# Performance work log

Measured on AMD Instinct MI355X. Metric: run time of the kernel, lower is better.

## Reference

```python
import jax, jax.numpy as jnp
import numpy as np

B, N, D, E, HEADS, HID = 8, 2048, 768, 4, 12, 3072
CAPF = 0.25
CAP = int(CAPF * N)  # 512 tokens per expert
DH = D // HEADS
EPS = 1e-5  # torch LayerNorm default
SCALE = 0.02


def _nested_masks(dim, n_exp):
    # expert e keeps the first dim // 2**e features (nested experts, MoNE)
    m = np.zeros((n_exp, dim), np.float32)
    for e in range(n_exp):
        m[e, : dim >> e] = 1.0
    return jnp.asarray(m)


def _ln(x, g, b):
    mu = x.mean(-1, keepdims=True)
    var = ((x - mu) ** 2).mean(-1, keepdims=True)
    return (x - mu) * jax.lax.rsqrt(var + EPS) * g + b


def setup_inputs() -> dict:
    key = jax.random.key(0)
    ks = jax.random.split(key, 8)
    return {
        "x": jax.random.normal(ks[0], (B, N, D), jnp.float32),
        "Wr": jax.random.normal(ks[1], (D, E), jnp.float32) * SCALE,
        "ln1_g": jnp.ones((D,), jnp.float32),
        "ln1_b": jnp.zeros((D,), jnp.float32),
        "ln2_g": jnp.ones((D,), jnp.float32),
        "ln2_b": jnp.zeros((D,), jnp.float32),
        "Wqkv": jax.random.normal(ks[2], (D, 3 * D), jnp.float32) * SCALE,
        "Wproj": jax.random.normal(ks[3], (D, D), jnp.float32) * SCALE,
        "bproj": jnp.zeros((D,), jnp.float32),
        "W1": jax.random.normal(ks[4], (D, HID), jnp.float32) * SCALE,
        "b1": jnp.zeros((HID,), jnp.float32),
        "W2": jax.random.normal(ks[5], (HID, D), jnp.float32) * SCALE,
        "b2": jnp.zeros((D,), jnp.float32),
    }


def reference(x, Wr, ln1_g, ln1_b, ln2_g, ln2_b, Wqkv, Wproj, bproj, W1, b1, W2, b2):
    mD = _nested_masks(D, E)[None, :, None, :]    # [1,E,1,D]
    mH = _nested_masks(HID, E)[None, :, None, :]  # [1,E,1,HID]

    # ---- expert-choice router ----
    probs = jax.nn.softmax(x @ Wr, axis=-1)                     # [B,N,E]
    gates, idx = jax.lax.top_k(probs.transpose(0, 2, 1), CAP)   # each [B,E,C]
    dispatch = jax.nn.one_hot(idx, N, dtype=x.dtype)            # [B,E,C,N]
    combine = dispatch * gates[..., None]                       # [B,E,C,N]

    # ---- attention branch (per-expert nested-masked attention) ----
    xn = _ln(x, ln1_g, ln1_b)
    xe = jnp.einsum('becn,bnd->becd', dispatch, xn)             # [B,E,C,D]
    qkv = (xe * mD) @ Wqkv                                      # input-masked linear
    q, k, v = jnp.split(qkv, 3, axis=-1)
    q, k, v = q * mD, k * mD, v * mD                            # nested output masks

    def to_heads(t):
        return t.reshape(B, E, CAP, HEADS, DH).transpose(0, 1, 3, 2, 4)  # [B,E,H,C,dh]

    q, k, v = to_heads(q), to_heads(k), to_heads(v)
    att = jax.nn.softmax(jnp.einsum('behcd,behkd->behck', q, k) * (DH ** -0.5), axis=-1)
    o = jnp.einsum('behck,behkd->behcd', att, v)
    o = o.transpose(0, 1, 3, 2, 4).reshape(B, E, CAP, D)
    ye = ((o @ Wproj) + bproj) * mD                             # masked proj
    x = x + jnp.einsum('becd,becn->bnd', ye, combine)           # combine back

    # ---- MLP branch (per-expert nested-masked MLP) ----
    xn2 = _ln(x, ln2_g, ln2_b)
    xe2 = jnp.einsum('becn,bnd->becd', dispatch, xn2)           # [B,E,C,D]
    h = jax.nn.gelu((((xe2 * mD) @ W1) + b1) * mH)              # [B,E,C,HID]
    y = ((h @ W2) + b2) * mD                                    # [B,E,C,D]
    x = x + jnp.einsum('becd,becn->bnd', y, combine)
    return x
```

## Files before the change

kernel.cpp:

```cpp
#include <hip/hip_runtime.h>
#include <stdint.h>

typedef uint16_t u16;
typedef uint32_t u32;
typedef uint64_t u64;
typedef float f32x4 __attribute__((ext_vector_type(4)));
typedef __bf16 bf16x8 __attribute__((ext_vector_type(8)));

#define DEVI __device__ __forceinline__

struct U4 { u32 a, b, c, d; };

DEVI u16 f2bf(float f) {
    u32 u = __builtin_bit_cast(u32, f);
    return (u16)((u + 0x7FFFu + ((u >> 16) & 1u)) >> 16);
}
DEVI float bf2f(u32 h) { return __builtin_bit_cast(float, h << 16); }
DEVI u32 cvt_pk_bf16(float lo, float hi) {
    u32 r;
    asm("v_cvt_pk_bf16_f32 %0, %1, %2" : "=v"(r) : "v"(lo), "v"(hi));
    return r;
}

DEVI float gelu_f(float x) {
    float u = 0.7978845608028654f * (x + 0.044715f * x * x * x);
    float t = exp2f(u * 2.885390081777927f);
    return x * (1.f - 1.f / (t + 1.f));
}

#define GLOAD_LDS16(gp, lp) \
    __builtin_amdgcn_global_load_lds((const __attribute__((address_space(1))) void*)(gp), \
                                     (__attribute__((address_space(3))) void*)(lp), 16, 0, 0)

struct WtJobs {
    const float* src[4]; u16* dst[4];
    int K[4], N[4], ntx[4], start[5];
};
__global__ __launch_bounds__(256) void wt_all_kernel(WtJobs a) {
    int j = 0;
#pragma unroll
    for (int k = 1; k < 4; k++) if ((int)blockIdx.x >= a.start[k]) j = k;
    const int local = blockIdx.x - a.start[j];
    const int N = a.N[j], K = a.K[j];
    const int n0 = (local % a.ntx[j]) * 32, k0 = (local / a.ntx[j]) * 32;
    const float* __restrict__ src = a.src[j];
    u16* __restrict__ dst = a.dst[j];
    __shared__ float tile[32][33];
    int tx = threadIdx.x & 31, ty = threadIdx.x >> 5;
#pragma unroll
    for (int i = 0; i < 32; i += 8)
        tile[ty + i][tx] = src[(size_t)(k0 + ty + i) * N + n0 + tx];
    __syncthreads();
#pragma unroll
    for (int i = 0; i < 32; i += 8)
        dst[(size_t)(n0 + ty + i) * K + k0 + tx] = f2bf(tile[tx][ty + i]);
}

__global__ __launch_bounds__(256) void routerln_kernel(const float* __restrict__ x,
                                                       const float* __restrict__ Wr,
                                                       const float* __restrict__ gw,
                                                       const float* __restrict__ bw,
                                                       float* __restrict__ probs,
                                                       u16* __restrict__ xn) {
    int wv = threadIdx.x >> 6, lane = threadIdx.x & 63;
    size_t t = (size_t)blockIdx.x * 4 + wv;
    const float4* xr = (const float4*)(x + t * 768);
    const float4* wr4 = (const float4*)Wr;
    float4 v[3]; float s = 0, s2 = 0, a0 = 0, a1 = 0, a2 = 0, a3 = 0;
#pragma unroll
    for (int i = 0; i < 3; i++) {
        int f4 = lane + 64 * i;
        v[i] = xr[f4];
        s += v[i].x + v[i].y + v[i].z + v[i].w;
        s2 += v[i].x * v[i].x + v[i].y * v[i].y + v[i].z * v[i].z + v[i].w * v[i].w;
#pragma unroll
        for (int jj = 0; jj < 4; jj++) {
            float xv = (jj == 0) ? v[i].x : (jj == 1) ? v[i].y : (jj == 2) ? v[i].z : v[i].w;
            float4 w = wr4[f4 * 4 + jj];
            a0 = fmaf(xv, w.x, a0); a1 = fmaf(xv, w.y, a1);
            a2 = fmaf(xv, w.z, a2); a3 = fmaf(xv, w.w, a3);
        }
    }
#pragma unroll
    for (int m = 1; m < 64; m <<= 1) {
        s += __shfl_xor(s, m); s2 += __shfl_xor(s2, m);
        a0 += __shfl_xor(a0, m); a1 += __shfl_xor(a1, m);
        a2 += __shfl_xor(a2, m); a3 += __shfl_xor(a3, m);
    }
    float mx = fmaxf(fmaxf(a0, a1), fmaxf(a2, a3));
    float e0 = expf(a0 - mx), e1 = expf(a1 - mx), e2 = expf(a2 - mx), e3 = expf(a3 - mx);
    float inv = 1.f / (e0 + e1 + e2 + e3);
    if (lane < 4) {
        float pv = (lane == 0) ? e0 : (lane == 1) ? e1 : (lane == 2) ? e2 : e3;
        int b = (int)(t >> 11), n = (int)(t & 2047);
        probs[(size_t)(b * 4 + lane) * 2048 + n] = pv * inv;
    }
    float mu = s * (1.f / 768.f);
    float var = s2 * (1.f / 768.f) - mu * mu;
    float rs = rsqrtf(var + 1e-5f);
    uint2* op = (uint2*)(xn + t * 768);
#pragma unroll
    for (int i = 0; i < 3; i++) {
        int j4 = (lane + 64 * i) * 4;
        float y0 = (v[i].x - mu) * rs * gw[j4 + 0] + bw[j4 + 0];
        float y1 = (v[i].y - mu) * rs * gw[j4 + 1] + bw[j4 + 1];
        float y2 = (v[i].z - mu) * rs * gw[j4 + 2] + bw[j4 + 2];
        float y3 = (v[i].w - mu) * rs * gw[j4 + 3] + bw[j4 + 3];
        uint2 o; o.x = cvt_pk_bf16(y0, y1); o.y = cvt_pk_bf16(y2, y3);
        op[lane + 64 * i] = o;
    }
}

__global__ __launch_bounds__(1024) void topk_kernel(const float* __restrict__ probs,
                                                    int* __restrict__ idx, float* __restrict__ gate,
                                                    int* __restrict__ rev) {
    int be = blockIdx.x; int b = be >> 2, e = be & 3;
    __shared__ u64 keys[2048];
    for (int n = threadIdx.x; n < 2048; n += 1024) {
        u32 p = __builtin_bit_cast(u32, probs[(size_t)be * 2048 + n]);
        keys[n] = ((u64)p << 32) | (u32)(2047 - n);
        rev[((size_t)b * 2048 + n) * 4 + e] = -1;
    }
    __syncthreads();
    for (int k = 2; k <= 2048; k <<= 1)
        for (int j = k >> 1; j > 0; j >>= 1) {
            for (int i = threadIdx.x; i < 2048; i += 1024) {
                int ixj = i ^ j;
                if (ixj > i) {
                    u64 a = keys[i], bb = keys[ixj];
                    bool up = ((i & k) == 0);
                    if (up ? (a < bb) : (a > bb)) { keys[i] = bb; keys[ixj] = a; }
                }
            }
            __syncthreads();
        }
    for (int c = threadIdx.x; c < 512; c += 1024) {
        u64 kk = keys[c];
        int n = 2047 - (int)(kk & 0xffffffffu);
        idx[be * 512 + c] = n;
        gate[be * 512 + c] = __builtin_bit_cast(float, (u32)(kk >> 32));
        rev[((size_t)b * 2048 + n) * 4 + e] = c;
    }
}

struct GemmJobs {
    const u16* A[4]; u16* C[4]; u16* VT[4]; const int* idx[4];
    const u16* BT; const float* bias;
    long sAb[4], sCb[4], sVb[4];
    int lda[4], ldc[4], nk[4], nmask[4], tps[4], tstart[4];
    int ldb;
};

template <int MODE>
__global__ __launch_bounds__(256) void gemm_kernel(GemmJobs a) {
    __shared__ __align__(16) char smem[2][16384];
    const int tid = threadIdx.x, wv = tid >> 6, lane = tid & 63;
    const int mt = blockIdx.y, bz = blockIdx.z;
    int e = 0;
#pragma unroll
    for (int k = 1; k < 4; k++) if ((int)blockIdx.x >= a.tstart[k]) e = k;
    const int local = blockIdx.x - a.tstart[e];
    int seg, ntl;
    if (MODE == 0) { seg = local / a.tps[e]; ntl = local - seg * a.tps[e]; }
    else { seg = 0; ntl = local; }
    const int nbase = seg * 768 + ntl * 128;
    const int lda = a.lda[e], ldc = a.ldc[e], nk = a.nk[e], nmask = a.nmask[e];
    const u16* Ap = a.A[e] + (long)bz * a.sAb[e];
    const int* ix = a.idx[e] ? (a.idx[e] + bz * 2048) : nullptr;

    auto stage = [&](int buf, int kt) {
        char* base = smem[buf] + ((wv >= 2) ? 8192 : 0);
        const int kb = kt * 32;
#pragma unroll
        for (int q = 0; q < 4; q++) {
            int i8 = (wv & 1) * 4 + q;
            int row = i8 * 16 + (lane >> 2);
            int clog = ((lane & 3) * 16) ^ ((row & 6) << 3);
            const u16* g;
            if (wv < 2) {
                int rs = ix ? ix[mt * 128 + row] : (mt * 128 + row);
                g = Ap + (long)rs * lda + kb;
            } else {
                g = a.BT + (long)(nbase + row) * a.ldb + kb;
            }
            GLOAD_LDS16((const char*)g + clog, base + i8 * 1024);
        }
    };

    f32x4 acc[4][4] = {};
    stage(0, 0);
    __syncthreads();
    int buf = 0;
    const int wr = wv >> 1, wc = wv & 1;
    const int cb = (lane >> 4) * 16;
    for (int kt = 0; kt < nk; kt++) {
        if (kt + 1 < nk) stage(buf ^ 1, kt + 1);
        const char* ab = smem[buf];
        const char* bb = smem[buf] + 8192;
        bf16x8 af[4], bfv[4];
#pragma unroll
        for (int mi = 0; mi < 4; mi++) {
            int r = wr * 64 + mi * 16 + (lane & 15);
            af[mi] = *(const bf16x8*)(ab + r * 64 + (cb ^ ((r & 6) << 3)));
        }
#pragma unroll
        for (int ni = 0; ni < 4; ni++) {
            int r = wc * 64 + ni * 16 + (lane & 15);
            bfv[ni] = *(const bf16x8*)(bb + r * 64 + (cb ^ ((r & 6) << 3)));
        }
#pragma unroll
        for (int mi = 0; mi < 4; mi++)
#pragma unroll
            for (int ni = 0; ni < 4; ni++)
                acc[mi][ni] = __builtin_amdgcn_mfma_f32_16x16x32_bf16(af[mi], bfv[ni], acc[mi][ni], 0, 0, 0);
        __syncthreads();
        buf ^= 1;
    }

    u16* Cb = a.C[e] + (long)bz * a.sCb[e];
    u16* Vb = (MODE == 0) ? (a.VT[e] + (long)bz * a.sVb[e]) : nullptr;
#pragma unroll
    for (int mi = 0; mi < 4; mi++) {
        const int r0 = mt * 128 + wr * 64 + mi * 16 + ((lane >> 4) << 2);
#pragma unroll
        for (int ni = 0; ni < 4; ni++) {
            const int colt = wc * 64 + ni * 16 + (lane & 15);
            const int nloc = ntl * 128 + colt;
            if (MODE == 0) {
                const bool act = nloc < nmask;
                if (seg < 2) {
                    u16* cp = Cb + (long)r0 * 1536 + seg * 768 + nloc;
#pragma unroll
                    for (int j = 0; j < 4; j++) cp[(long)j * 1536] = act ? f2bf(acc[mi][ni][j]) : (u16)0;
                } else {
                    uint2 pv;
                    if (act) { pv.x = cvt_pk_bf16(acc[mi][ni][0], acc[mi][ni][1]);
                               pv.y = cvt_pk_bf16(acc[mi][ni][2], acc[mi][ni][3]); }
                    else { pv.x = 0; pv.y = 0; }
                    *(uint2*)(Vb + (long)nloc * 512 + r0) = pv;
                }
            } else {
                const float bv = a.bias[nloc];
#pragma unroll
                for (int j = 0; j < 4; j++) {
                    float v = acc[mi][ni][j] + bv;
                    if (MODE == 2) v = gelu_f(v);
                    Cb[(long)(r0 + j) * ldc + nloc] = f2bf(v);
                }
            }
        }
    }
}

__global__ __launch_bounds__(256) void attn_kernel(const u16* __restrict__ qkv,
                                                   const u16* __restrict__ vt,
                                                   u16* __restrict__ obuf) {
    const int qt = blockIdx.x, hj = blockIdx.y, b = blockIdx.z;
    int e, h;
    if (hj < 12) { e = 0; h = hj; }
    else if (hj < 18) { e = 1; h = hj - 12; }
    else if (hj < 21) { e = 2; h = hj - 18; }
    else { e = 3; h = hj - 21; }
    const int job = b * 4 + e;
    const u16* qkvj = qkv + (size_t)job * 512 * 1536;
    const u16* vtj = vt + (size_t)job * 768 * 512 + (size_t)h * 64 * 512;
    u16* oj = obuf + (size_t)job * 512 * 768;
    __shared__ __align__(16) char lds[32768];
    char* Klds = lds;
    char* Vlds = lds + 16384;
    const int tid = threadIdx.x, wv = tid >> 6;
    const int lane = tid & 63, l15 = lane & 15, lg = lane >> 4;
    const int q0 = qt * 128 + wv * 32;

    bf16x8 qf[2][2];
#pragma unroll
    for (int n2 = 0; n2 < 2; n2++)
#pragma unroll
        for (int ks = 0; ks < 2; ks++)
            qf[n2][ks] = *(const bf16x8*)(qkvj + (size_t)(q0 + n2 * 16 + l15) * 1536 + h * 64 + ks * 32 + lg * 8);

    uint4 kreg[4], vreg[4];
    const int fr = tid >> 3, fch = tid & 7;
    const int fdl = tid >> 4, fcv = tid & 15;
    auto issue = [&](int t) {
        const int kv0 = t * 128;
#pragma unroll
        for (int ii = 0; ii < 4; ii++) {
            kreg[ii] = *(const uint4*)(qkvj + (size_t)(kv0 + fr + 32 * ii) * 1536 + 768 + h * 64 + fch * 8);
            vreg[ii] = *(const uint4*)(vtj + (size_t)(fdl + 16 * ii) * 512 + kv0 + fcv * 8);
        }
    };

    f32x4 oacc[4][2] = {};
    float mrun[2] = {-1e30f, -1e30f}, lrun[2] = {0.f, 0.f};
    const float SA = 0.18033688011112042f;

    issue(0);
    for (int t = 0; t < 4; t++) {
        __syncthreads();
#pragma unroll
        for (int ii = 0; ii < 4; ii++) {
            int r = fr + 32 * ii;
            *(uint4*)(Klds + r * 128 + ((fch * 16) ^ ((r & 7) << 4))) = kreg[ii];
            int dl = fdl + 16 * ii;
            *(uint4*)(Vlds + dl * 256 + ((fcv * 16) ^ ((dl & 7) << 4))) = vreg[ii];
        }
        __syncthreads();
        if (t < 3) issue(t + 1);

        f32x4 sacc[8][2] = {};
#pragma unroll
        for (int ks = 0; ks < 2; ks++)
#pragma unroll
            for (int m8 = 0; m8 < 8; m8++) {
                int r = m8 * 16 + l15;
                bf16x8 kf = *(const bf16x8*)(Klds + r * 128 + ((ks * 64 + lg * 16) ^ ((r & 7) << 4)));
#pragma unroll
                for (int n2 = 0; n2 < 2; n2++)
                    sacc[m8][n2] = __builtin_amdgcn_mfma_f32_16x16x32_bf16(kf, qf[n2][ks], sacc[m8][n2], 0, 0, 0);
            }

        u32 pk[8][2][2];
#pragma unroll
        for (int n2 = 0; n2 < 2; n2++) {
            float pm[8];
#pragma unroll
            for (int m8 = 0; m8 < 8; m8++)
                pm[m8] = fmaxf(fmaxf(sacc[m8][n2][0], sacc[m8][n2][1]),
                               fmaxf(sacc[m8][n2][2], sacc[m8][n2][3]));
            float tm = fmaxf(fmaxf(fmaxf(pm[0], pm[1]), fmaxf(pm[2], pm[3])),
                             fmaxf(fmaxf(pm[4], pm[5]), fmaxf(pm[6], pm[7])));
            tm = fmaxf(tm, __shfl_xor(tm, 16));
            tm = fmaxf(tm, __shfl_xor(tm, 32));
            float mnew = fmaxf(mrun[n2], tm);
            float alpha = exp2f((mrun[n2] - mnew) * SA);
            float ps[8];
#pragma unroll
            for (int m8 = 0; m8 < 8; m8++) {
#pragma unroll
                for (int j = 0; j < 4; j++)
                    sacc[m8][n2][j] = exp2f((sacc[m8][n2][j] - mnew) * SA);
                ps[m8] = (sacc[m8][n2][0] + sacc[m8][n2][1]) + (sacc[m8][n2][2] + sacc[m8][n2][3]);
            }
            float tsum = ((ps[0] + ps[1]) + (ps[2] + ps[3])) + ((ps[4] + ps[5]) + (ps[6] + ps[7]));
            tsum += __shfl_xor(tsum, 16);
            tsum += __shfl_xor(tsum, 32);
            lrun[n2] = lrun[n2] * alpha + tsum;
            mrun[n2] = mnew;
#pragma unroll
            for (int mo = 0; mo < 4; mo++) oacc[mo][n2] *= alpha;
#pragma unroll
            for (int m8 = 0; m8 < 8; m8++) {
                pk[m8][n2][0] = cvt_pk_bf16(sacc[m8][n2][0], sacc[m8][n2][1]);
                pk[m8][n2][1] = cvt_pk_bf16(sacc[m8][n2][2], sacc[m8][n2][3]);
            }
        }

        const int la = ((2 * lg) & 3) * 16 + l15;
        const int lb = ((2 * lg + 1) & 3) * 16 + l15;
#pragma unroll
        for (int kb = 0; kb < 4; kb++) {
            bf16x8 pb[2];
#pragma unroll
            for (int n2 = 0; n2 < 2; n2++) {
                u32 w[4];
#pragma unroll
                for (int half = 0; half < 2; half++) {
                    int src = (half == 0) ? la : lb;
                    u32 aA = (u32)__shfl((int)pk[2 * kb + 0][n2][0], src);
                    u32 aB = (u32)__shfl((int)pk[2 * kb + 1][n2][0], src);
                    u32 bA = (u32)__shfl((int)pk[2 * kb + 0][n2][1], src);
                    u32 bB = (u32)__shfl((int)pk[2 * kb + 1][n2][1], src);
                    w[half * 2 + 0] = (lg < 2) ? aA : aB;
                    w[half * 2 + 1] = (lg < 2) ? bA : bB;
                }
                U4 uw{w[0], w[1], w[2], w[3]};
                pb[n2] = __builtin_bit_cast(bf16x8, uw);
            }
#pragma unroll
            for (int mo = 0; mo < 4; mo++) {
                int r = mo * 16 + l15;
                bf16x8 vf = *(const bf16x8*)(Vlds + r * 256 + ((kb * 64 + lg * 16) ^ ((r & 7) << 4)));
#pragma unroll
                for (int n2 = 0; n2 < 2; n2++)
                    oacc[mo][n2] = __builtin_amdgcn_mfma_f32_16x16x32_bf16(vf, pb[n2], oacc[mo][n2], 0, 0, 0);
            }
        }
    }

#pragma unroll
    for (int n2 = 0; n2 < 2; n2++) {
        float inv = 1.f / lrun[n2];
        int c = q0 + n2 * 16 + l15;
#pragma unroll
        for (int mo = 0; mo < 4; mo++) {
            uint2 o;
            o.x = cvt_pk_bf16(oacc[mo][n2][0] * inv, oacc[mo][n2][1] * inv);
            o.y = cvt_pk_bf16(oacc[mo][n2][2] * inv, oacc[mo][n2][3] * inv);
            *(uint2*)(oj + (size_t)c * 768 + h * 64 + mo * 16 + lg * 4) = o;
        }
    }
}

template <int DO_LN>
__global__ __launch_bounds__(256) void combineln_kernel(const float* __restrict__ basex,
                                                        float* __restrict__ outp,
                                                        const u16* __restrict__ ye,
                                                        const int* __restrict__ rev,
                                                        const float* __restrict__ gate,
                                                        const float* __restrict__ gw,
                                                        const float* __restrict__ bw,
                                                        u16* __restrict__ xn) {
    int wv = threadIdx.x >> 6, lane = threadIdx.x & 63;
    size_t t = (size_t)blockIdx.x * 4 + wv;
    const int b = (int)(t >> 11);
    const int4 rv = *(const int4*)(rev + t * 4);
    const int cs[4] = {rv.x, rv.y, rv.z, rv.w};
    float4 v[3];
#pragma unroll
    for (int i = 0; i < 3; i++) v[i] = *(const float4*)(basex + t * 768 + (lane + 64 * i) * 4);
#pragma unroll
    for (int e = 0; e < 4; e++) {
        const int c = cs[e];
        if (c >= 0) {
            const int job = b * 4 + e;
            const float g = gate[job * 512 + c];
            const u16* yr = ye + ((size_t)job * 512 + c) * 768;
#pragma unroll
            for (int i = 0; i < 3; i++) {
                int f4 = lane + 64 * i;
                if (f4 < (192 >> e)) {
                    uint2 raw = *(const uint2*)(yr + f4 * 4);
                    v[i].x += g * bf2f(raw.x & 0xffffu);
                    v[i].y += g * bf2f(raw.x >> 16);
                    v[i].z += g * bf2f(raw.y & 0xffffu);
                    v[i].w += g * bf2f(raw.y >> 16);
                }
            }
        }
    }
#pragma unroll
    for (int i = 0; i < 3; i++) *(float4*)(outp + t * 768 + (lane + 64 * i) * 4) = v[i];
    if (DO_LN) {
        float s = 0, s2 = 0;
#pragma unroll
        for (int i = 0; i < 3; i++) {
            s += v[i].x + v[i].y + v[i].z + v[i].w;
            s2 += v[i].x * v[i].x + v[i].y * v[i].y + v[i].z * v[i].z + v[i].w * v[i].w;
        }
#pragma unroll
        for (int m = 1; m < 64; m <<= 1) { s += __shfl_xor(s, m); s2 += __shfl_xor(s2, m); }
        float mu = s * (1.f / 768.f);
        float var = s2 * (1.f / 768.f) - mu * mu;
        float rs = rsqrtf(var + 1e-5f);
        uint2* op = (uint2*)(xn + t * 768);
#pragma unroll
        for (int i = 0; i < 3; i++) {
            int j4 = (lane + 64 * i) * 4;
            float y0 = (v[i].x - mu) * rs * gw[j4 + 0] + bw[j4 + 0];
            float y1 = (v[i].y - mu) * rs * gw[j4 + 1] + bw[j4 + 1];
            float y2 = (v[i].z - mu) * rs * gw[j4 + 2] + bw[j4 + 2];
            float y3 = (v[i].w - mu) * rs * gw[j4 + 3] + bw[j4 + 3];
            uint2 o; o.x = cvt_pk_bf16(y0, y1); o.y = cvt_pk_bf16(y2, y3);
            op[lane + 64 * i] = o;
        }
    }
}

extern "C" void kernel_launch(void* const* d_in, const int* in_sizes, int n_in,
                              void* d_out, int out_size, void* d_ws, size_t ws_size,
                              hipStream_t stream) {
    (void)in_sizes; (void)n_in; (void)out_size; (void)ws_size;
    const float* x     = (const float*)d_in[0];
    const float* Wr    = (const float*)d_in[1];
    const float* ln1g  = (const float*)d_in[2];
    const float* ln1b  = (const float*)d_in[3];
    const float* ln2g  = (const float*)d_in[4];
    const float* ln2b  = (const float*)d_in[5];
    const float* Wqkv  = (const float*)d_in[6];
    const float* Wproj = (const float*)d_in[7];
    const float* bproj = (const float*)d_in[8];
    const float* W1    = (const float*)d_in[9];
    const float* b1    = (const float*)d_in[10];
    const float* W2    = (const float*)d_in[11];
    const float* b2    = (const float*)d_in[12];
    float* outp = (float*)d_out;

    char* ws = (char*)d_ws;
    size_t off = 0;
    auto take = [&](size_t bytes) -> void* {
        void* p = ws + off;
        off += (bytes + 255) & ~(size_t)255;
        return p;
    };
    u16*   WqkvT  = (u16*)take((size_t)2304 * 768 * 2);
    u16*   WprojT = (u16*)take((size_t)768 * 768 * 2);
    u16*   W1T    = (u16*)take((size_t)3072 * 768 * 2);
    u16*   W2T    = (u16*)take((size_t)768 * 3072 * 2);
    float* probs  = (float*)take((size_t)32 * 2048 * 4);
    int*   idxb   = (int*)take((size_t)32 * 512 * 4);
    float* gateb  = (float*)take((size_t)32 * 512 * 4);
    int*   revb   = (int*)take((size_t)8 * 2048 * 4 * 4);
    u16*   xn     = (u16*)take((size_t)8 * 2048 * 768 * 2);
    u16*   qkvb   = (u16*)take((size_t)32 * 512 * 1536 * 2);
    u16*   vtb    = (u16*)take((size_t)32 * 768 * 512 * 2);
    u16*   ob     = (u16*)take((size_t)32 * 512 * 768 * 2);
    u16*   yeb    = (u16*)take((size_t)32 * 512 * 768 * 2);
    u16*   hb     = qkvb;

    const int Dk_[4] = {768, 384, 192, 96};
    const int He_[4] = {3072, 1536, 768, 384};
    size_t eoffH[4];
    { size_t s = 0; for (int e = 0; e < 4; e++) { eoffH[e] = s; s += (size_t)8 * 512 * He_[e]; } }

    WtJobs wj{};
    wj.src[0] = Wqkv;  wj.dst[0] = WqkvT;  wj.K[0] = 768;  wj.N[0] = 2304;
    wj.src[1] = Wproj; wj.dst[1] = WprojT; wj.K[1] = 768;  wj.N[1] = 768;
    wj.src[2] = W1;    wj.dst[2] = W1T;    wj.K[2] = 768;  wj.N[2] = 3072;
    wj.src[3] = W2;    wj.dst[3] = W2T;    wj.K[3] = 3072; wj.N[3] = 768;
    { int s = 0; for (int j = 0; j < 4; j++) { wj.ntx[j] = wj.N[j] / 32; wj.start[j] = s; s += (wj.N[j] / 32) * (wj.K[j] / 32); } wj.start[4] = s;
      wt_all_kernel<<<s, 256, 0, stream>>>(wj); }

    routerln_kernel<<<4096, 256, 0, stream>>>(x, Wr, ln1g, ln1b, probs, xn);
    topk_kernel<<<32, 1024, 0, stream>>>(probs, idxb, gateb, revb);

    {
        GemmJobs ga{};
        ga.BT = WqkvT; ga.bias = nullptr; ga.ldb = 768;
        int s = 0;
        for (int e = 0; e < 4; e++) {
            int tps = (Dk_[e] + 127) / 128;
            ga.A[e] = xn; ga.C[e] = qkvb + (size_t)e * 512 * 1536; ga.VT[e] = vtb + (size_t)e * 768 * 512;
            ga.idx[e] = idxb + e * 512;
            ga.sAb[e] = (long)2048 * 768; ga.sCb[e] = (long)4 * 512 * 1536; ga.sVb[e] = (long)4 * 768 * 512;
            ga.lda[e] = 768; ga.ldc[e] = 1536; ga.nk[e] = Dk_[e] / 32; ga.nmask[e] = Dk_[e];
            ga.tps[e] = tps; ga.tstart[e] = s; s += 3 * tps;
        }
        gemm_kernel<0><<<dim3(s, 4, 8), 256, 0, stream>>>(ga);
    }

    attn_kernel<<<dim3(4, 23, 8), 256, 0, stream>>>(qkvb, vtb, ob);

    {
        GemmJobs ga{};
        ga.BT = WprojT; ga.bias = bproj; ga.ldb = 768;
        int s = 0;
        for (int e = 0; e < 4; e++) {
            int tps = (Dk_[e] + 127) / 128;
            ga.A[e] = ob + (size_t)e * 512 * 768; ga.C[e] = yeb + (size_t)e * 512 * 768;
            ga.VT[e] = nullptr; ga.idx[e] = nullptr;
            ga.sAb[e] = (long)4 * 512 * 768; ga.sCb[e] = (long)4 * 512 * 768; ga.sVb[e] = 0;
            ga.lda[e] = 768; ga.ldc[e] = 768; ga.nk[e] = Dk_[e] / 32; ga.nmask[e] = 768;
            ga.tps[e] = tps; ga.tstart[e] = s; s += tps;
        }
        gemm_kernel<1><<<dim3(s, 4, 8), 256, 0, stream>>>(ga);
    }

    combineln_kernel<1><<<4096, 256, 0, stream>>>(x, outp, yeb, revb, gateb, ln2g, ln2b, xn);

    {
        GemmJobs ga{};
        ga.BT = W1T; ga.bias = b1; ga.ldb = 768;
        int s = 0;
        for (int e = 0; e < 4; e++) {
            ga.A[e] = xn; ga.C[e] = hb + eoffH[e]; ga.VT[e] = nullptr; ga.idx[e] = idxb + e * 512;
            ga.sAb[e] = (long)2048 * 768; ga.sCb[e] = (long)512 * He_[e]; ga.sVb[e] = 0;
            ga.lda[e] = 768; ga.ldc[e] = He_[e]; ga.nk[e] = Dk_[e] / 32; ga.nmask[e] = He_[e];
            ga.tps[e] = He_[e] / 128; ga.tstart[e] = s; s += He_[e] / 128;
        }
        gemm_kernel<2><<<dim3(s, 4, 8), 256, 0, stream>>>(ga);
    }
    {
        GemmJobs ga{};
        ga.BT = W2T; ga.bias = b2; ga.ldb = 3072;
        int s = 0;
        for (int e = 0; e < 4; e++) {
            int tps = (Dk_[e] + 127) / 128;
            ga.A[e] = hb + eoffH[e]; ga.C[e] = yeb + (size_t)e * 512 * 768;
            ga.VT[e] = nullptr; ga.idx[e] = nullptr;
            ga.sAb[e] = (long)512 * He_[e]; ga.sCb[e] = (long)4 * 512 * 768; ga.sVb[e] = 0;
            ga.lda[e] = He_[e]; ga.ldc[e] = 768; ga.nk[e] = He_[e] / 32; ga.nmask[e] = 768;
            ga.tps[e] = tps; ga.tstart[e] = s; s += tps;
        }
        gemm_kernel<1><<<dim3(s, 4, 8), 256, 0, stream>>>(ga);
    }

    combineln_kernel<0><<<4096, 256, 0, stream>>>(outp, outp, yeb, revb, gateb, nullptr, nullptr, nullptr);
}
```

Before: 516.0 us.

## Swap MFMA operands for row-contiguous GEMM stores and stage attention output via LDS

In the GEMM, row-major outputs now come from MFMAs with the A and B operands swapped, so each lane holds four consecutive columns. This allows packed 8-byte stores and a float4 bias load in place of scalar strided 2-byte stores. The attention epilogue writes each wave's output tile into a swizzled LDS buffer, then reads it back and emits 16-byte coalesced global stores. The attention grid is also flattened to 1D with the query tile as the slowest-varying index, which changes block scheduling order.

```diff
diff --git a/kernel.cpp b/kernel.cpp
--- a/kernel.cpp
+++ b/kernel.cpp
@@ -167,6 +167,7 @@
     const int lda = a.lda[e], ldc = a.ldc[e], nk = a.nk[e], nmask = a.nmask[e];
     const u16* Ap = a.A[e] + (long)bz * a.sAb[e];
     const int* ix = a.idx[e] ? (a.idx[e] + bz * 2048) : nullptr;
+    const bool swapped = (MODE != 0) || (seg < 2);
 
     auto stage = [&](int buf, int kt) {
         char* base = smem[buf] + ((wv >= 2) ? 8192 : 0);
@@ -192,7 +193,8 @@
     __syncthreads();
     int buf = 0;
     const int wr = wv >> 1, wc = wv & 1;
-    const int cb = (lane >> 4) * 16;
+    const int l15 = lane & 15, lg = lane >> 4;
+    const int cb = lg * 16;
     for (int kt = 0; kt < nk; kt++) {
         if (kt + 1 < nk) stage(buf ^ 1, kt + 1);
         const char* ab = smem[buf];
@@ -200,53 +202,77 @@
         bf16x8 af[4], bfv[4];
 #pragma unroll
         for (int mi = 0; mi < 4; mi++) {
-            int r = wr * 64 + mi * 16 + (lane & 15);
+            int r = wr * 64 + mi * 16 + l15;
             af[mi] = *(const bf16x8*)(ab + r * 64 + (cb ^ ((r & 6) << 3)));
         }
 #pragma unroll
         for (int ni = 0; ni < 4; ni++) {
-            int r = wc * 64 + ni * 16 + (lane & 15);
+            int r = wc * 64 + ni * 16 + l15;
             bfv[ni] = *(const bf16x8*)(bb + r * 64 + (cb ^ ((r & 6) << 3)));
         }
-#pragma unroll
-        for (int mi = 0; mi < 4; mi++)
-#pragma unroll
-            for (int ni = 0; ni < 4; ni++)
-                acc[mi][ni] = __builtin_amdgcn_mfma_f32_16x16x32_bf16(af[mi], bfv[ni], acc[mi][ni], 0, 0, 0);
+        if (swapped) {
+#pragma unroll
+            for (int mi = 0; mi < 4; mi++)
+#pragma unroll
+                for (int ni = 0; ni < 4; ni++)
+                    acc[mi][ni] = __builtin_amdgcn_mfma_f32_16x16x32_bf16(bfv[ni], af[mi], acc[mi][ni], 0, 0, 0);
+        } else {
+#pragma unroll
+            for (int mi = 0; mi < 4; mi++)
+#pragma unroll
+                for (int ni = 0; ni < 4; ni++)
+                    acc[mi][ni] = __builtin_amdgcn_mfma_f32_16x16x32_bf16(af[mi], bfv[ni], acc[mi][ni], 0, 0, 0);
+        }
         __syncthreads();
         buf ^= 1;
     }
 
     u16* Cb = a.C[e] + (long)bz * a.sCb[e];
-    u16* Vb = (MODE == 0) ? (a.VT[e] + (long)bz * a.sVb[e]) : nullptr;
-#pragma unroll
-    for (int mi = 0; mi < 4; mi++) {
-        const int r0 = mt * 128 + wr * 64 + mi * 16 + ((lane >> 4) << 2);
-#pragma unroll
-        for (int ni = 0; ni < 4; ni++) {
-            const int colt = wc * 64 + ni * 16 + (lane & 15);
-            const int nloc = ntl * 128 + colt;
-            if (MODE == 0) {
+    if (MODE == 0 && seg == 2) {
+        u16* Vb = a.VT[e] + (long)bz * a.sVb[e];
+#pragma unroll
+        for (int mi = 0; mi < 4; mi++) {
+            const int r0 = mt * 128 + wr * 64 + mi * 16 + (lg << 2);
+#pragma unroll
+            for (int ni = 0; ni < 4; ni++) {
+                const int nloc = ntl * 128 + wc * 64 + ni * 16 + l15;
                 const bool act = nloc < nmask;
-                if (seg < 2) {
-                    u16* cp = Cb + (long)r0 * 1536 + seg * 768 + nloc;
-#pragma unroll
-                    for (int j = 0; j < 4; j++) cp[(long)j * 1536] = act ? f2bf(acc[mi][ni][j]) : (u16)0;
-                } else {
-                    uint2 pv;
-                    if (act) { pv.x = cvt_pk_bf16(acc[mi][ni][0], acc[mi][ni][1]);
-                               pv.y = cvt_pk_bf16(acc[mi][ni][2], acc[mi][ni][3]); }
-                    else { pv.x = 0; pv.y = 0; }
-                    *(uint2*)(Vb + (long)nloc * 512 + r0) = pv;
-                }
-            } else {
-                const float bv = a.bias[nloc];
-#pragma unroll
-                for (int j = 0; j < 4; j++) {
-                    float v = acc[mi][ni][j] + bv;
-                    if (MODE == 2) v = gelu_f(v);
-                    Cb[(long)(r0 + j) * ldc + nloc] = f2bf(v);
-                }
+                uint2 pv;
+                if (act) { pv.x = cvt_pk_bf16(acc[mi][ni][0], acc[mi][ni][1]);
+                           pv.y = cvt_pk_bf16(acc[mi][ni][2], acc[mi][ni][3]); }
+                else { pv.x = 0; pv.y = 0; }
+                *(uint2*)(Vb + (long)nloc * 512 + r0) = pv;
+            }
+        }
+    } else if (MODE == 0) {
+#pragma unroll
+        for (int mi = 0; mi < 4; mi++) {
+            const int row = mt * 128 + wr * 64 + mi * 16 + l15;
+            u16* cp = Cb + (long)row * 1536 + seg * 768 + ntl * 128;
+#pragma unroll
+            for (int ni = 0; ni < 4; ni++) {
+                const int colb = wc * 64 + ni * 16 + lg * 4;
+                const bool act = (ntl * 128 + colb) < nmask;
+                uint2 pv;
+                if (act) { pv.x = cvt_pk_bf16(acc[mi][ni][0], acc[mi][ni][1]);
+                           pv.y = cvt_pk_bf16(acc[mi][ni][2], acc[mi][ni][3]); }
+                else { pv.x = 0; pv.y = 0; }
+                *(uint2*)(cp + colb) = pv;
+            }
+        }
+    } else {
+#pragma unroll
+        for (int mi = 0; mi < 4; mi++) {
+            const int row = mt * 128 + wr * 64 + mi * 16 + l15;
+#pragma unroll
+            for (int ni = 0; ni < 4; ni++) {
+                const int nloc = ntl * 128 + wc * 64 + ni * 16 + lg * 4;
+                const float4 bv = *(const float4*)(a.bias + nloc);
+                float v0 = acc[mi][ni][0] + bv.x, v1 = acc[mi][ni][1] + bv.y;
+                float v2 = acc[mi][ni][2] + bv.z, v3 = acc[mi][ni][3] + bv.w;
+                if (MODE == 2) { v0 = gelu_f(v0); v1 = gelu_f(v1); v2 = gelu_f(v2); v3 = gelu_f(v3); }
+                uint2 pv; pv.x = cvt_pk_bf16(v0, v1); pv.y = cvt_pk_bf16(v2, v3);
+                *(uint2*)(Cb + (long)row * ldc + nloc) = pv;
             }
         }
     }
@@ -255,7 +281,10 @@
 __global__ __launch_bounds__(256) void attn_kernel(const u16* __restrict__ qkv,
                                                    const u16* __restrict__ vt,
                                                    u16* __restrict__ obuf) {
-    const int qt = blockIdx.x, hj = blockIdx.y, b = blockIdx.z;
+    const int bid = blockIdx.x;
+    const int jobl = bid % 184;
+    const int qt = bid / 184;
+    const int b = jobl / 23, hj = jobl % 23;
     int e, h;
     if (hj < 12) { e = 0; h = hj; }
     else if (hj < 18) { e = 1; h = hj - 12; }
@@ -388,17 +417,30 @@
         }
     }
 
+    __syncthreads();
+    char* Wl = lds + wv * 4096;
 #pragma unroll
     for (int n2 = 0; n2 < 2; n2++) {
         float inv = 1.f / lrun[n2];
-        int c = q0 + n2 * 16 + l15;
+        int c = n2 * 16 + l15;
 #pragma unroll
         for (int mo = 0; mo < 4; mo++) {
+            int tch = mo * 2 + (lg >> 1);
+            int byteoff = c * 128 + (((tch ^ (c & 7)) << 4)) + (lg & 1) * 8;
             uint2 o;
             o.x = cvt_pk_bf16(oacc[mo][n2][0] * inv, oacc[mo][n2][1] * inv);
             o.y = cvt_pk_bf16(oacc[mo][n2][2] * inv, oacc[mo][n2][3] * inv);
-            *(uint2*)(oj + (size_t)c * 768 + h * 64 + mo * 16 + lg * 4) = o;
-        }
+            *(uint2*)(Wl + byteoff) = o;
+        }
+    }
+    asm volatile("s_waitcnt lgkmcnt(0)" ::: "memory");
+    __builtin_amdgcn_sched_barrier(0);
+#pragma unroll
+    for (int p = 0; p < 4; p++) {
+        int row = p * 8 + (lane >> 3);
+        int tch = lane & 7;
+        uint4 v = *(const uint4*)(Wl + row * 128 + ((tch ^ (row & 7)) << 4));
+        *(uint4*)(oj + (size_t)(q0 + row) * 768 + h * 64 + tch * 8) = v;
     }
 }
 
@@ -539,7 +581,7 @@
         gemm_kernel<0><<<dim3(s, 4, 8), 256, 0, stream>>>(ga);
     }
 
-    attn_kernel<<<dim3(4, 23, 8), 256, 0, stream>>>(qkvb, vtb, ob);
+    attn_kernel<<<736, 256, 0, stream>>>(qkvb, vtb, ob);
 
     {
         GemmJobs ga{};
```

Result: no change. 525.4 us (+1.8%).
